# Optimization experiments

Hardware: AMD Instinct MI355X
Metric: run time of the kernel (lower is better)

Reference implementation:

```python
import jax, jax.numpy as jnp
import numpy as np

B, N, IC, PC, OUT = 2, 4096, 256, 128, 128
BN_EPS = 1e-5


def setup_inputs() -> dict:
    key = jax.random.key(0)
    ks = jax.random.split(key, 6)
    return {
        "point_features": jax.random.normal(ks[0], (B, PC, N), jnp.float32),
        "img_features": jax.random.normal(ks[1], (B, IC, N), jnp.float32),
        "fc2_w": jax.random.normal(ks[2], (PC, IC), jnp.float32) * (1.0 / np.sqrt(IC)),
        "fc2_b": jax.random.normal(ks[3], (PC,), jnp.float32) * 0.01,
        "conv_w": jax.random.normal(ks[4], (OUT, 2 * PC), jnp.float32) * (1.0 / np.sqrt(2 * PC)),
        "conv_b": jax.random.normal(ks[5], (OUT,), jnp.float32) * 0.01,
        "bn_gamma": jnp.ones((OUT,), jnp.float32),
        "bn_beta": jnp.zeros((OUT,), jnp.float32),
        "bn_mean": jnp.zeros((OUT,), jnp.float32),
        "bn_var": jnp.ones((OUT,), jnp.float32),
    }


def reference(point_features, img_features, fc2_w, fc2_b, conv_w, conv_b,
              bn_gamma, bn_beta, bn_mean, bn_var):
    # IA_layer3 (dropout in eval mode -> identity)
    rp = jnp.swapaxes(point_features, 1, 2)            # [B, N, pc]
    ri = jnp.swapaxes(img_features, 1, 2) @ fc2_w.T + fc2_b  # fc2: [B, N, pc]
    scale = 1.0 / np.sqrt(PC).astype(np.float32)

    # scores = rp @ ri^T / sqrt(d); softmax over dim=1 (the rp-token axis)
    s_p = jnp.einsum('bnd,bmd->bnm', rp, ri) * scale   # [B, N, N]
    aw_p = jax.nn.softmax(s_p, axis=1)
    out_p = jnp.einsum('bij,bjd->bid', aw_p, rp)       # [B, N, pc]

    s_i = jnp.einsum('bnd,bmd->bnm', ri, rp) * scale   # [B, N, N]
    aw_i = jax.nn.softmax(s_i, axis=1)
    out_i = jnp.einsum('bij,bjd->bid', aw_i, ri)       # [B, N, pc]

    # fuse: permute to channel-first, concat on channels -> [B, 2*pc, N]
    fusion = jnp.concatenate([jnp.swapaxes(out_p, 1, 2),
                              jnp.swapaxes(out_i, 1, 2)], axis=1)
    # conv1d(k=1) + BN(eval) + ReLU, all per-channel elementwise over N
    y = jnp.einsum('oc,bcn->bon', conv_w, fusion) + conv_b[None, :, None]
    inv_std = jax.lax.rsqrt(bn_var + BN_EPS)
    y = (y - bn_mean[None, :, None]) * (bn_gamma * inv_std)[None, :, None] \
        + bn_beta[None, :, None]
    return jax.nn.relu(y)                              # [B, OUT, N]
```

## Files before the change

### kernel.cpp

```cpp
#include <hip/hip_runtime.h>
#include <math.h>

#define NTOK 4096
#define PCH  128
#define ICH  256
#define OCH  128
#define NB   2
#define SCALEF 0.08838834764831845f

typedef __bf16 bf16_t;
typedef __attribute__((ext_vector_type(8))) __bf16 bf16x8;
typedef __attribute__((ext_vector_type(4))) __bf16 bf16x4;
typedef __attribute__((ext_vector_type(4))) float floatx4;

#define LDK 136
#define LDJ 72

__global__ __launch_bounds__(256) void zero_kernel(float4* __restrict__ p)
{
    p[(size_t)blockIdx.x * 256 + threadIdx.x] = float4{0.f, 0.f, 0.f, 0.f};
}

__global__ __launch_bounds__(256) void pack_pf(const float* __restrict__ pf,
                                               bf16_t* __restrict__ pfC,
                                               bf16_t* __restrict__ pfT)
{
    __shared__ float Ls[64][65];
    const int t = threadIdx.x;
    const int n0 = blockIdx.x * 64, d0 = blockIdx.y * 64, b = blockIdx.z;
    const float* src = pf + ((size_t)(b * PCH + d0)) * NTOK + n0;
#pragma unroll
    for (int p = 0; p < 4; p++) {
        int d = p * 16 + (t >> 4), c = t & 15;
        float4 v = *(const float4*)&src[d * NTOK + c * 4];
        Ls[d][c * 4 + 0] = v.x; Ls[d][c * 4 + 1] = v.y;
        Ls[d][c * 4 + 2] = v.z; Ls[d][c * 4 + 3] = v.w;
        bf16x4 o = { (bf16_t)v.x, (bf16_t)v.y, (bf16_t)v.z, (bf16_t)v.w };
        *(bf16x4*)&pfC[((size_t)(b * PCH + d0 + d)) * NTOK + n0 + c * 4] = o;
    }
    __syncthreads();
#pragma unroll
    for (int p = 0; p < 2; p++) {
        int n = p * 32 + (t >> 3), c = t & 7;
        bf16x8 o;
#pragma unroll
        for (int k = 0; k < 8; k++) o[k] = (bf16_t)Ls[c * 8 + k][n];
        *(bf16x8*)&pfT[((size_t)(b * NTOK + n0 + n)) * PCH + d0 + c * 8] = o;
    }
}

__global__ __launch_bounds__(256) void fc2_kernel(const float* __restrict__ img,
                                                  const float* __restrict__ w,
                                                  const float* __restrict__ bias,
                                                  bf16_t* __restrict__ riC,
                                                  bf16_t* __restrict__ riT)
{
    const int b = blockIdx.z, t = threadIdx.x;
    const int n = blockIdx.x * 64 + (t & 63);
    const int pbase = blockIdx.y * 32 + (t >> 6) * 8;
    const float* imgb = img + (size_t)b * ICH * NTOK + n;

    float acc[8];
#pragma unroll
    for (int pp = 0; pp < 8; pp++) acc[pp] = bias[pbase + pp];

    for (int c = 0; c < ICH; c += 4) {
        float v0 = imgb[(c + 0) * NTOK];
        float v1 = imgb[(c + 1) * NTOK];
        float v2 = imgb[(c + 2) * NTOK];
        float v3 = imgb[(c + 3) * NTOK];
#pragma unroll
        for (int pp = 0; pp < 8; pp++) {
            float4 wv = *(const float4*)&w[(pbase + pp) * ICH + c];
            acc[pp] += wv.x * v0 + wv.y * v1 + wv.z * v2 + wv.w * v3;
        }
    }

#pragma unroll
    for (int pp = 0; pp < 8; pp++)
        riC[((size_t)(b * PCH + pbase + pp)) * NTOK + n] = (bf16_t)acc[pp];
    bf16x8 tv;
#pragma unroll
    for (int pp = 0; pp < 8; pp++) tv[pp] = (bf16_t)acc[pp];
    *(bf16x8*)&riT[((size_t)(b * NTOK + n)) * PCH + pbase] = tv;
}

__global__ __launch_bounds__(256, 4) void stats_mfma(const bf16_t* __restrict__ pfT,
                                                     const bf16_t* __restrict__ riT,
                                                     float* __restrict__ zr,
                                                     float* __restrict__ zc)
{
    __shared__ bf16_t As[64 * LDK];
    __shared__ float zacc[1024];
    const int b = blockIdx.y, t = threadIdx.x;
    const int js = blockIdx.z;
    const bf16_t* At = pfT + (size_t)b * NTOK * PCH;
    const bf16_t* Bt = riT + (size_t)b * NTOK * PCH;
    float* zrow = zr + (size_t)b * NTOK;
    float* zcol = zc + (size_t)b * NTOK;
    const int lane = t & 63, w = t >> 6, tx = lane & 15, q = lane >> 4;
    const int i0 = blockIdx.x * 64;
    const int jbase = js * 1024;
    const int sr = t >> 4, sc = t & 15;
    const bf16_t* Brow = Bt + (size_t)(jbase + w * 16 + tx) * PCH;

    bf16x8 bcur[4];
#pragma unroll
    for (int s = 0; s < 4; s++)
        bcur[s] = *(const bf16x8*)&Brow[s * 32 + q * 8];
#pragma unroll
    for (int p = 0; p < 4; p++) {
        int i = p * 16 + sr;
        *(uint4*)&As[i * LDK + sc * 8] = *(const uint4*)&At[((size_t)(i0 + i)) * PCH + sc * 8];
    }
    __syncthreads();
    bf16x8 af[4][4];
#pragma unroll
    for (int mt = 0; mt < 4; mt++)
#pragma unroll
        for (int s = 0; s < 4; s++)
            af[mt][s] = *(bf16x8*)&As[(mt * 16 + tx) * LDK + s * 32 + q * 8];

    float racc[4] = {0.f, 0.f, 0.f, 0.f};
    for (int jt = 0; jt < 16; jt++) {
        __builtin_amdgcn_s_barrier();
        floatx4 sacc[4];
#pragma unroll
        for (int mt = 0; mt < 4; mt++) {
            sacc[mt] = (floatx4){0.f, 0.f, 0.f, 0.f};
#pragma unroll
            for (int s = 0; s < 4; s++)
                sacc[mt] = __builtin_amdgcn_mfma_f32_16x16x32_bf16(bcur[s], af[mt][s], sacc[mt], 0, 0, 0);
        }
        if (jt < 15) {
            const bf16_t* bn = Brow + (size_t)(jt + 1) * 64 * PCH;
#pragma unroll
            for (int s = 0; s < 4; s++)
                bcur[s] = *(const bf16x8*)&bn[s * 32 + q * 8];
        }

        float ctmp[4] = {0.f, 0.f, 0.f, 0.f};
#pragma unroll
        for (int mt = 0; mt < 4; mt++)
#pragma unroll
            for (int r = 0; r < 4; r++) {
                float e = __expf(sacc[mt][r] * SCALEF);
                racc[mt] += e;
                ctmp[r]  += e;
            }
#pragma unroll
        for (int r = 0; r < 4; r++) {
            float v = ctmp[r];
            v += __shfl_xor(v, 1); v += __shfl_xor(v, 2);
            v += __shfl_xor(v, 4); v += __shfl_xor(v, 8);
            if (tx == 0) zacc[jt * 64 + w * 16 + q * 4 + r] = v;
        }
    }
#pragma unroll
    for (int mt = 0; mt < 4; mt++) {
        float v = racc[mt];
        v += __shfl_xor(v, 16);
        v += __shfl_xor(v, 32);
        if (q == 0) atomicAdd(&zrow[i0 + mt * 16 + tx], v);
    }
    __syncthreads();
#pragma unroll
    for (int k = 0; k < 4; k++)
        atomicAdd(&zcol[jbase + k * 256 + t], zacc[k * 256 + t]);
}

__global__ __launch_bounds__(256, 3) void attn_mfma(const bf16_t* __restrict__ pfT,
                                                    const bf16_t* __restrict__ riT,
                                                    const bf16_t* __restrict__ pfC,
                                                    const bf16_t* __restrict__ riC,
                                                    const float* __restrict__ zrsum,
                                                    const float* __restrict__ zcsum,
                                                    float* __restrict__ fus)
{
    __shared__ bf16_t As[64 * LDK];
    __shared__ bf16_t Es[2][64 * LDJ];
    const int b = blockIdx.y, t = threadIdx.x;
    const int mode = blockIdx.z >> 2, js = blockIdx.z & 3;
    const bf16_t* At = (mode == 0 ? pfT : riT) + (size_t)b * NTOK * PCH;
    const bf16_t* Bt = (mode == 0 ? riT : pfT) + (size_t)b * NTOK * PCH;
    const bf16_t* Vc = (mode == 0 ? pfC : riC) + (size_t)b * PCH * NTOK;
    const float* wsum = (mode == 0 ? zcsum : zrsum) + (size_t)b * NTOK;
    const int lane = t & 63, w = t >> 6, tx = lane & 15, q = lane >> 4;
    const int i0 = blockIdx.x * 64;
    const int jbase = js * 1024;
    const int sr = t >> 4, sc = t & 15;
    const bf16_t* Brow = Bt + (size_t)(jbase + w * 16 + tx) * PCH;

    bf16x8 bcur[4];
#pragma unroll
    for (int s = 0; s < 4; s++)
        bcur[s] = *(const bf16x8*)&Brow[s * 32 + q * 8];
    bf16x8 vcur[2][2];
#pragma unroll
    for (int nt = 0; nt < 2; nt++)
#pragma unroll
        for (int s = 0; s < 2; s++)
            vcur[nt][s] = *(const bf16x8*)&Vc[((size_t)(w * 32 + nt * 16 + tx)) * NTOK + jbase + s * 32 + q * 8];
    float4 wv = *(const float4*)&wsum[jbase + w * 16 + q * 4];
    float4 wr4 = {1.f / wv.x, 1.f / wv.y, 1.f / wv.z, 1.f / wv.w};

#pragma unroll
    for (int p = 0; p < 4; p++) {
        int i = p * 16 + sr;
        *(uint4*)&As[i * LDK + sc * 8] = *(const uint4*)&At[((size_t)(i0 + i)) * PCH + sc * 8];
    }
    __syncthreads();
    bf16x8 af[4][4];
#pragma unroll
    for (int mt = 0; mt < 4; mt++)
#pragma unroll
        for (int s = 0; s < 4; s++)
            af[mt][s] = *(bf16x8*)&As[(mt * 16 + tx) * LDK + s * 32 + q * 8];

    floatx4 outacc[4][2];
#pragma unroll
    for (int mt = 0; mt < 4; mt++)
#pragma unroll
        for (int nt = 0; nt < 2; nt++)
            outacc[mt][nt] = (floatx4){0.f, 0.f, 0.f, 0.f};

    for (int jt = 0; jt < 16; jt++) {
        const int cur = jt & 1;
        const int j0 = jbase + jt * 64;

        floatx4 sacc[4];
#pragma unroll
        for (int mt = 0; mt < 4; mt++) {
            sacc[mt] = (floatx4){0.f, 0.f, 0.f, 0.f};
#pragma unroll
            for (int s = 0; s < 4; s++)
                sacc[mt] = __builtin_amdgcn_mfma_f32_16x16x32_bf16(bcur[s], af[mt][s], sacc[mt], 0, 0, 0);
        }
        if (jt < 15) {
            const bf16_t* bn = Brow + (size_t)(jt + 1) * 64 * PCH;
#pragma unroll
            for (int s = 0; s < 4; s++)
                bcur[s] = *(const bf16x8*)&bn[s * 32 + q * 8];
        }

#pragma unroll
        for (int mt = 0; mt < 4; mt++) {
            bf16x4 ev;
#pragma unroll
            for (int r = 0; r < 4; r++)
                ev[r] = (bf16_t)(__expf(sacc[mt][r] * SCALEF) * ((const float*)&wr4)[r]);
            *(bf16x4*)&Es[cur][(mt * 16 + tx) * LDJ + w * 16 + q * 4] = ev;
        }
        float4 wnv;
        if (jt < 15)
            wnv = *(const float4*)&wsum[j0 + 64 + w * 16 + q * 4];

        __syncthreads();

        bf16x8 ef[4][2];
#pragma unroll
        for (int mt = 0; mt < 4; mt++)
#pragma unroll
            for (int s = 0; s < 2; s++)
                ef[mt][s] = *(bf16x8*)&Es[cur][(mt * 16 + tx) * LDJ + s * 32 + q * 8];
#pragma unroll
        for (int nt = 0; nt < 2; nt++)
#pragma unroll
            for (int s = 0; s < 2; s++)
#pragma unroll
                for (int mt = 0; mt < 4; mt++)
                    outacc[mt][nt] = __builtin_amdgcn_mfma_f32_16x16x32_bf16(ef[mt][s], vcur[nt][s], outacc[mt][nt], 0, 0, 0);

        if (jt < 15) {
#pragma unroll
            for (int nt = 0; nt < 2; nt++)
#pragma unroll
                for (int s = 0; s < 2; s++)
                    vcur[nt][s] = *(const bf16x8*)&Vc[((size_t)(w * 32 + nt * 16 + tx)) * NTOK + (j0 + 64) + s * 32 + q * 8];
            wr4 = (float4){1.f / wnv.x, 1.f / wnv.y, 1.f / wnv.z, 1.f / wnv.w};
        }
    }

    float* fo = fus + ((size_t)(b * NTOK + i0)) * 256 + mode * 128 + w * 32;
#pragma unroll
    for (int mt = 0; mt < 4; mt++)
#pragma unroll
        for (int nt = 0; nt < 2; nt++)
#pragma unroll
            for (int r = 0; r < 4; r++)
                atomicAdd(&fo[(mt * 16 + q * 4 + r) * 256 + nt * 16 + tx], outacc[mt][nt][r]);
}

__global__ __launch_bounds__(256) void conv_kernel(const float* __restrict__ fus,
                                                   const float* __restrict__ cw,
                                                   const float* __restrict__ cb,
                                                   const float* __restrict__ g,
                                                   const float* __restrict__ be,
                                                   const float* __restrict__ mu,
                                                   const float* __restrict__ var,
                                                   float* __restrict__ out)
{
    __shared__ float Ls[64][260];
    const int b = blockIdx.z, t = threadIdx.x;
    const int n0 = blockIdx.x * 64;
    const int obase = blockIdx.y * 32 + (t >> 6) * 8;

    const float4* src = (const float4*)(fus + ((size_t)(b * NTOK + n0)) * 256);
#pragma unroll
    for (int it = 0; it < 16; it++) {
        int row = it * 4 + (t >> 6);
        float4 v = src[row * 64 + (t & 63)];
        *(float4*)&Ls[row][(t & 63) * 4] = v;
    }
    __syncthreads();

    const int n = t & 63;
    float acc[8] = {};
    for (int c = 0; c < 256; c += 4) {
        float4 v = *(const float4*)&Ls[n][c];
#pragma unroll
        for (int oo = 0; oo < 8; oo++) {
            float4 wv = *(const float4*)&cw[(obase + oo) * 256 + c];
            acc[oo] += wv.x * v.x + wv.y * v.y + wv.z * v.z + wv.w * v.w;
        }
    }
#pragma unroll
    for (int oo = 0; oo < 8; oo++) {
        const int o = obase + oo;
        const float s  = g[o] * rsqrtf(var[o] + 1e-5f);
        const float b0 = be[o] + (cb[o] - mu[o]) * s;
        float y = acc[oo] * s + b0;
        out[((size_t)(b * OCH + o)) * NTOK + n0 + n] = fmaxf(y, 0.f);
    }
}

extern "C" void kernel_launch(void* const* d_in, const int* in_sizes, int n_in,
                              void* d_out, int out_size, void* d_ws, size_t ws_size,
                              hipStream_t stream)
{
    const float* pf   = (const float*)d_in[0];
    const float* img  = (const float*)d_in[1];
    const float* fc2w = (const float*)d_in[2];
    const float* fc2b = (const float*)d_in[3];
    const float* cw   = (const float*)d_in[4];
    const float* cb   = (const float*)d_in[5];
    const float* g    = (const float*)d_in[6];
    const float* be   = (const float*)d_in[7];
    const float* mu   = (const float*)d_in[8];
    const float* var  = (const float*)d_in[9];
    float* out = (float*)d_out;

    float* fus   = (float*)d_ws;
    float* zrsum = fus + (size_t)NB * NTOK * 256;
    float* zcsum = zrsum + NB * NTOK;
    bf16_t* pfC = (bf16_t*)(zcsum + NB * NTOK);
    bf16_t* pfT = pfC + (size_t)NB * PCH * NTOK;
    bf16_t* riC = pfT + (size_t)NB * NTOK * PCH;
    bf16_t* riT = riC + (size_t)NB * PCH * NTOK;

    zero_kernel<<<dim3(2064), 256, 0, stream>>>((float4*)d_ws);
    pack_pf    <<<dim3(64, 2, NB),  256, 0, stream>>>(pf, pfC, pfT);
    fc2_kernel <<<dim3(64, 4, NB),  256, 0, stream>>>(img, fc2w, fc2b, riC, riT);
    stats_mfma <<<dim3(64, NB, 4),  256, 0, stream>>>(pfT, riT, zrsum, zcsum);
    attn_mfma  <<<dim3(64, NB, 8),  256, 0, stream>>>(pfT, riT, pfC, riC, zrsum, zcsum, fus);
    conv_kernel<<<dim3(64, 4, NB),  256, 0, stream>>>(fus, cw, cb, g, be, mu, var, out);
}
```

Baseline: 249.3 us.

## Software-pipeline score computation one tile ahead of PV accumulation

Restructures the attention inner loop so the score MFMAs and exp for tile jt+1 are computed and written to the alternate LDS buffer while the PV MFMAs for tile jt run. A prologue computes the first tile, and the barrier moves to the end of each iteration. The aim is to overlap the exp/convert latency with matrix work and give the scheduler independent MFMA streams. In exchange it raises register pressure and adds prefetch-distance bookkeeping for B rows and wsum.

```diff
diff --git a/kernel.cpp b/kernel.cpp
--- a/kernel.cpp
+++ b/kernel.cpp
@@ -224,10 +224,7 @@
         for (int nt = 0; nt < 2; nt++)
             outacc[mt][nt] = (floatx4){0.f, 0.f, 0.f, 0.f};
 
-    for (int jt = 0; jt < 16; jt++) {
-        const int cur = jt & 1;
-        const int j0 = jbase + jt * 64;
-
+    {
         floatx4 sacc[4];
 #pragma unroll
         for (int mt = 0; mt < 4; mt++) {
@@ -236,26 +233,26 @@
             for (int s = 0; s < 4; s++)
                 sacc[mt] = __builtin_amdgcn_mfma_f32_16x16x32_bf16(bcur[s], af[mt][s], sacc[mt], 0, 0, 0);
         }
-        if (jt < 15) {
-            const bf16_t* bn = Brow + (size_t)(jt + 1) * 64 * PCH;
-#pragma unroll
-            for (int s = 0; s < 4; s++)
-                bcur[s] = *(const bf16x8*)&bn[s * 32 + q * 8];
-        }
-
+        const bf16_t* bn = Brow + (size_t)64 * PCH;
+#pragma unroll
+        for (int s = 0; s < 4; s++)
+            bcur[s] = *(const bf16x8*)&bn[s * 32 + q * 8];
+        float4 wnv = *(const float4*)&wsum[jbase + 64 + w * 16 + q * 4];
 #pragma unroll
         for (int mt = 0; mt < 4; mt++) {
             bf16x4 ev;
 #pragma unroll
             for (int r = 0; r < 4; r++)
                 ev[r] = (bf16_t)(__expf(sacc[mt][r] * SCALEF) * ((const float*)&wr4)[r]);
-            *(bf16x4*)&Es[cur][(mt * 16 + tx) * LDJ + w * 16 + q * 4] = ev;
-        }
-        float4 wnv;
-        if (jt < 15)
-            wnv = *(const float4*)&wsum[j0 + 64 + w * 16 + q * 4];
-
-        __syncthreads();
+            *(bf16x4*)&Es[0][(mt * 16 + tx) * LDJ + w * 16 + q * 4] = ev;
+        }
+        wr4 = (float4){1.f / wnv.x, 1.f / wnv.y, 1.f / wnv.z, 1.f / wnv.w};
+    }
+    __syncthreads();
+
+    for (int jt = 0; jt < 16; jt++) {
+        const int cur = jt & 1, nxt = cur ^ 1;
+        const int j0 = jbase + jt * 64;
 
         bf16x8 ef[4][2];
 #pragma unroll
@@ -263,6 +260,32 @@
 #pragma unroll
             for (int s = 0; s < 2; s++)
                 ef[mt][s] = *(bf16x8*)&Es[cur][(mt * 16 + tx) * LDJ + s * 32 + q * 8];
+
+        if (jt < 15) {
+            floatx4 sacc[4];
+#pragma unroll
+            for (int mt = 0; mt < 4; mt++) {
+                sacc[mt] = (floatx4){0.f, 0.f, 0.f, 0.f};
+#pragma unroll
+                for (int s = 0; s < 4; s++)
+                    sacc[mt] = __builtin_amdgcn_mfma_f32_16x16x32_bf16(bcur[s], af[mt][s], sacc[mt], 0, 0, 0);
+            }
+            if (jt < 14) {
+                const bf16_t* bn = Brow + (size_t)(jt + 2) * 64 * PCH;
+#pragma unroll
+                for (int s = 0; s < 4; s++)
+                    bcur[s] = *(const bf16x8*)&bn[s * 32 + q * 8];
+            }
+#pragma unroll
+            for (int mt = 0; mt < 4; mt++) {
+                bf16x4 ev;
+#pragma unroll
+                for (int r = 0; r < 4; r++)
+                    ev[r] = (bf16_t)(__expf(sacc[mt][r] * SCALEF) * ((const float*)&wr4)[r]);
+                *(bf16x4*)&Es[nxt][(mt * 16 + tx) * LDJ + w * 16 + q * 4] = ev;
+            }
+        }
+
 #pragma unroll
         for (int nt = 0; nt < 2; nt++)
 #pragma unroll
@@ -272,13 +295,18 @@
                     outacc[mt][nt] = __builtin_amdgcn_mfma_f32_16x16x32_bf16(ef[mt][s], vcur[nt][s], outacc[mt][nt], 0, 0, 0);
 
         if (jt < 15) {
+            float4 wnv;
+            if (jt < 14)
+                wnv = *(const float4*)&wsum[j0 + 128 + w * 16 + q * 4];
 #pragma unroll
             for (int nt = 0; nt < 2; nt++)
 #pragma unroll
                 for (int s = 0; s < 2; s++)
                     vcur[nt][s] = *(const bf16x8*)&Vc[((size_t)(w * 32 + nt * 16 + tx)) * NTOK + (j0 + 64) + s * 32 + q * 8];
-            wr4 = (float4){1.f / wnv.x, 1.f / wnv.y, 1.f / wnv.z, 1.f / wnv.w};
-        }
+            if (jt < 14)
+                wr4 = (float4){1.f / wnv.x, 1.f / wnv.y, 1.f / wnv.z, 1.f / wnv.w};
+        }
+        __syncthreads();
     }
 
     float* fo = fus + ((size_t)(b * NTOK + i0)) * 256 + mode * 128 + w * 32;
```

Measured after the change: 265.6 us. 1.07x slower.

## Move fc2 and output conv projections onto bf16 MFMA

Applied to the files above, without the earlier changes.

Replaces the scalar FP32 fc2 and conv1d kernels with bf16 MFMA 16x16x32 kernels. fc2 first needs a new transpose/pack kernel that writes image features token-major in bf16 into the fusion workspace, and the zero kernel is moved after fc2 so that buffer can be reused. The aim is to cut the FMA-bound cost of the two projection stages. In exchange it adds an extra launch, converts the weights to bf16 on every load, and lowers the precision of both projections.

```diff
diff --git a/kernel.cpp b/kernel.cpp
--- a/kernel.cpp
+++ b/kernel.cpp
@@ -49,40 +49,74 @@
     }
 }
 
-__global__ __launch_bounds__(256) void fc2_kernel(const float* __restrict__ img,
-                                                  const float* __restrict__ w,
-                                                  const float* __restrict__ bias,
-                                                  bf16_t* __restrict__ riC,
-                                                  bf16_t* __restrict__ riT)
-{
-    const int b = blockIdx.z, t = threadIdx.x;
-    const int n = blockIdx.x * 64 + (t & 63);
-    const int pbase = blockIdx.y * 32 + (t >> 6) * 8;
-    const float* imgb = img + (size_t)b * ICH * NTOK + n;
-
-    float acc[8];
-#pragma unroll
-    for (int pp = 0; pp < 8; pp++) acc[pp] = bias[pbase + pp];
-
-    for (int c = 0; c < ICH; c += 4) {
-        float v0 = imgb[(c + 0) * NTOK];
-        float v1 = imgb[(c + 1) * NTOK];
-        float v2 = imgb[(c + 2) * NTOK];
-        float v3 = imgb[(c + 3) * NTOK];
-#pragma unroll
-        for (int pp = 0; pp < 8; pp++) {
-            float4 wv = *(const float4*)&w[(pbase + pp) * ICH + c];
-            acc[pp] += wv.x * v0 + wv.y * v1 + wv.z * v2 + wv.w * v3;
-        }
-    }
-
-#pragma unroll
-    for (int pp = 0; pp < 8; pp++)
-        riC[((size_t)(b * PCH + pbase + pp)) * NTOK + n] = (bf16_t)acc[pp];
-    bf16x8 tv;
-#pragma unroll
-    for (int pp = 0; pp < 8; pp++) tv[pp] = (bf16_t)acc[pp];
-    *(bf16x8*)&riT[((size_t)(b * NTOK + n)) * PCH + pbase] = tv;
+__global__ __launch_bounds__(256) void pack_img(const float* __restrict__ img,
+                                                bf16_t* __restrict__ imgT)
+{
+    __shared__ float Ls[64][65];
+    const int t = threadIdx.x;
+    const int n0 = blockIdx.x * 64, c0 = blockIdx.y * 64, b = blockIdx.z;
+    const float* src = img + ((size_t)(b * ICH + c0)) * NTOK + n0;
+#pragma unroll
+    for (int p = 0; p < 4; p++) {
+        int d = p * 16 + (t >> 4), c = t & 15;
+        float4 v = *(const float4*)&src[d * NTOK + c * 4];
+        Ls[d][c * 4 + 0] = v.x; Ls[d][c * 4 + 1] = v.y;
+        Ls[d][c * 4 + 2] = v.z; Ls[d][c * 4 + 3] = v.w;
+    }
+    __syncthreads();
+#pragma unroll
+    for (int p = 0; p < 2; p++) {
+        int n = p * 32 + (t >> 3), c = t & 7;
+        bf16x8 o;
+#pragma unroll
+        for (int k = 0; k < 8; k++) o[k] = (bf16_t)Ls[c * 8 + k][n];
+        *(bf16x8*)&imgT[((size_t)(b * NTOK + n0 + n)) * ICH + c0 + c * 8] = o;
+    }
+}
+
+__global__ __launch_bounds__(256) void fc2_mfma(const bf16_t* __restrict__ imgT,
+                                                const float* __restrict__ w,
+                                                const float* __restrict__ bias,
+                                                bf16_t* __restrict__ riC,
+                                                bf16_t* __restrict__ riT)
+{
+    const int t = threadIdx.x;
+    const int n0 = blockIdx.x * 64, pbase = blockIdx.y * 64, b = blockIdx.z;
+    const int lane = t & 63, wv = t >> 6, tx = lane & 15, q = lane >> 4;
+    const int n = n0 + wv * 16 + tx;
+    const bf16_t* trow = imgT + ((size_t)(b * NTOK + n)) * ICH;
+
+    floatx4 acc[4];
+#pragma unroll
+    for (int ot = 0; ot < 4; ot++) acc[ot] = (floatx4){0.f, 0.f, 0.f, 0.f};
+
+#pragma unroll
+    for (int s = 0; s < 8; s++) {
+        bf16x8 bf = *(const bf16x8*)&trow[s * 32 + q * 8];
+#pragma unroll
+        for (int ot = 0; ot < 4; ot++) {
+            const float* wr = w + (size_t)(pbase + ot * 16 + tx) * ICH + s * 32 + q * 8;
+            float4 x0 = *(const float4*)wr;
+            float4 x1 = *(const float4*)(wr + 4);
+            bf16x8 af;
+            af[0] = (bf16_t)x0.x; af[1] = (bf16_t)x0.y; af[2] = (bf16_t)x0.z; af[3] = (bf16_t)x0.w;
+            af[4] = (bf16_t)x1.x; af[5] = (bf16_t)x1.y; af[6] = (bf16_t)x1.z; af[7] = (bf16_t)x1.w;
+            acc[ot] = __builtin_amdgcn_mfma_f32_16x16x32_bf16(af, bf, acc[ot], 0, 0, 0);
+        }
+    }
+
+#pragma unroll
+    for (int ot = 0; ot < 4; ot++) {
+        bf16x4 tv;
+#pragma unroll
+        for (int r = 0; r < 4; r++) {
+            const int p = pbase + ot * 16 + q * 4 + r;
+            float v = acc[ot][r] + bias[p];
+            tv[r] = (bf16_t)v;
+            riC[((size_t)(b * PCH + p)) * NTOK + n] = (bf16_t)v;
+        }
+        *(bf16x4*)&riT[((size_t)(b * NTOK + n)) * PCH + pbase + ot * 16 + q * 4] = tv;
+    }
 }
 
 __global__ __launch_bounds__(256, 4) void stats_mfma(const bf16_t* __restrict__ pfT,
@@ -291,47 +325,54 @@
                 atomicAdd(&fo[(mt * 16 + q * 4 + r) * 256 + nt * 16 + tx], outacc[mt][nt][r]);
 }
 
-__global__ __launch_bounds__(256) void conv_kernel(const float* __restrict__ fus,
-                                                   const float* __restrict__ cw,
-                                                   const float* __restrict__ cb,
-                                                   const float* __restrict__ g,
-                                                   const float* __restrict__ be,
-                                                   const float* __restrict__ mu,
-                                                   const float* __restrict__ var,
-                                                   float* __restrict__ out)
-{
-    __shared__ float Ls[64][260];
-    const int b = blockIdx.z, t = threadIdx.x;
-    const int n0 = blockIdx.x * 64;
-    const int obase = blockIdx.y * 32 + (t >> 6) * 8;
-
-    const float4* src = (const float4*)(fus + ((size_t)(b * NTOK + n0)) * 256);
-#pragma unroll
-    for (int it = 0; it < 16; it++) {
-        int row = it * 4 + (t >> 6);
-        float4 v = src[row * 64 + (t & 63)];
-        *(float4*)&Ls[row][(t & 63) * 4] = v;
-    }
-    __syncthreads();
-
-    const int n = t & 63;
-    float acc[8] = {};
-    for (int c = 0; c < 256; c += 4) {
-        float4 v = *(const float4*)&Ls[n][c];
-#pragma unroll
-        for (int oo = 0; oo < 8; oo++) {
-            float4 wv = *(const float4*)&cw[(obase + oo) * 256 + c];
-            acc[oo] += wv.x * v.x + wv.y * v.y + wv.z * v.z + wv.w * v.w;
-        }
-    }
-#pragma unroll
-    for (int oo = 0; oo < 8; oo++) {
-        const int o = obase + oo;
-        const float s  = g[o] * rsqrtf(var[o] + 1e-5f);
-        const float b0 = be[o] + (cb[o] - mu[o]) * s;
-        float y = acc[oo] * s + b0;
-        out[((size_t)(b * OCH + o)) * NTOK + n0 + n] = fmaxf(y, 0.f);
-    }
+__global__ __launch_bounds__(256) void conv_mfma(const float* __restrict__ fus,
+                                                 const float* __restrict__ cw,
+                                                 const float* __restrict__ cb,
+                                                 const float* __restrict__ g,
+                                                 const float* __restrict__ be,
+                                                 const float* __restrict__ mu,
+                                                 const float* __restrict__ var,
+                                                 float* __restrict__ out)
+{
+    const int t = threadIdx.x;
+    const int n0 = blockIdx.x * 64, obase = blockIdx.y * 64, b = blockIdx.z;
+    const int lane = t & 63, wv = t >> 6, tx = lane & 15, q = lane >> 4;
+    const int n = n0 + wv * 16 + tx;
+    const float* frow = fus + ((size_t)(b * NTOK + n)) * 256;
+
+    floatx4 acc[4];
+#pragma unroll
+    for (int ot = 0; ot < 4; ot++) acc[ot] = (floatx4){0.f, 0.f, 0.f, 0.f};
+
+#pragma unroll
+    for (int s = 0; s < 8; s++) {
+        float4 f0 = *(const float4*)&frow[s * 32 + q * 8];
+        float4 f1 = *(const float4*)&frow[s * 32 + q * 8 + 4];
+        bf16x8 bf;
+        bf[0] = (bf16_t)f0.x; bf[1] = (bf16_t)f0.y; bf[2] = (bf16_t)f0.z; bf[3] = (bf16_t)f0.w;
+        bf[4] = (bf16_t)f1.x; bf[5] = (bf16_t)f1.y; bf[6] = (bf16_t)f1.z; bf[7] = (bf16_t)f1.w;
+#pragma unroll
+        for (int ot = 0; ot < 4; ot++) {
+            const float* wr = cw + (size_t)(obase + ot * 16 + tx) * 256 + s * 32 + q * 8;
+            float4 x0 = *(const float4*)wr;
+            float4 x1 = *(const float4*)(wr + 4);
+            bf16x8 af;
+            af[0] = (bf16_t)x0.x; af[1] = (bf16_t)x0.y; af[2] = (bf16_t)x0.z; af[3] = (bf16_t)x0.w;
+            af[4] = (bf16_t)x1.x; af[5] = (bf16_t)x1.y; af[6] = (bf16_t)x1.z; af[7] = (bf16_t)x1.w;
+            acc[ot] = __builtin_amdgcn_mfma_f32_16x16x32_bf16(af, bf, acc[ot], 0, 0, 0);
+        }
+    }
+
+#pragma unroll
+    for (int ot = 0; ot < 4; ot++)
+#pragma unroll
+        for (int r = 0; r < 4; r++) {
+            const int o = obase + ot * 16 + q * 4 + r;
+            const float sc = g[o] * rsqrtf(var[o] + 1e-5f);
+            const float b0 = be[o] + (cb[o] - mu[o]) * sc;
+            float y = acc[ot][r] * sc + b0;
+            out[((size_t)(b * OCH + o)) * NTOK + n] = fmaxf(y, 0.f);
+        }
 }
 
 extern "C" void kernel_launch(void* const* d_in, const int* in_sizes, int n_in,
@@ -357,11 +398,13 @@
     bf16_t* pfT = pfC + (size_t)NB * PCH * NTOK;
     bf16_t* riC = pfT + (size_t)NB * NTOK * PCH;
     bf16_t* riT = riC + (size_t)NB * PCH * NTOK;
-
+    bf16_t* imgT = (bf16_t*)fus;
+
+    pack_pf    <<<dim3(64, 2, NB),  256, 0, stream>>>(pf, pfC, pfT);
+    pack_img   <<<dim3(64, 4, NB),  256, 0, stream>>>(img, imgT);
+    fc2_mfma   <<<dim3(64, 2, NB),  256, 0, stream>>>(imgT, fc2w, fc2b, riC, riT);
     zero_kernel<<<dim3(2064), 256, 0, stream>>>((float4*)d_ws);
-    pack_pf    <<<dim3(64, 2, NB),  256, 0, stream>>>(pf, pfC, pfT);
-    fc2_kernel <<<dim3(64, 4, NB),  256, 0, stream>>>(img, fc2w, fc2b, riC, riT);
     stats_mfma <<<dim3(64, NB, 4),  256, 0, stream>>>(pfT, riT, zrsum, zcsum);
     attn_mfma  <<<dim3(64, NB, 8),  256, 0, stream>>>(pfT, riT, pfC, riC, zrsum, zcsum, fus);
-    conv_kernel<<<dim3(64, 4, NB),  256, 0, stream>>>(fus, cw, cb, g, be, mu, var, out);
-}
+    conv_mfma  <<<dim3(64, 2, NB),  256, 0, stream>>>(fus, cw, cb, g, be, mu, var, out);
+}
```

Result: faster. 214.1 us (-14.1%).
